# Kernel optimization log

Measured on AMD Instinct MI355X. Metric: run time of the kernel, lower is better.

The kernel has to match this reference:

```python
import jax, jax.numpy as jnp
import numpy as np
import math

D_MODEL = 1024
EXPAND = 2
D_INNER = EXPAND * D_MODEL        # 2048
HEADDIM = 64
NHEADS = D_INNER // HEADDIM       # 32
D_STATE = 128
D_CONV = 4
CHUNK = 128
SEQLEN = 4096
BATCH = 1                         # bidirectional merge in forward hard-codes batch=1
CONV_DIM = D_INNER + 2 * (2 * D_STATE)            # 2560
D_IN_PROJ = 2 * D_INNER + 2 * (2 * D_STATE) + 2 * NHEADS  # 4672
EPS = 1e-5


def silu(x):
    return x * jax.nn.sigmoid(x)


def segsum_exp(a):
    """exp(segsum(a)): out[..., i, j] = exp(sum_{k=j+1..i} a[..., k]) for i>=j else 0."""
    T = a.shape[-1]
    m1 = jnp.tril(jnp.ones((T, T), bool), -1)
    s = jnp.cumsum(jnp.where(m1, a[..., :, None], 0.0), axis=-2)
    m0 = jnp.tril(jnp.ones((T, T), bool))
    return jnp.where(m0, jnp.exp(jnp.where(m0, s, 0.0)), 0.0)


def ssd(x, A, B, C, chunk):
    """x:(b,L,h,p) A:(b,L,h) B,C:(b,L,n) (head dim of size 1 squeezed). L % chunk == 0."""
    b, L, h, p = x.shape
    c = L // chunk
    x = x.reshape(b, c, chunk, h, p)
    A = A.reshape(b, c, chunk, h).transpose(0, 3, 1, 2)   # (b,h,c,l)
    B = B.reshape(b, c, chunk, -1)
    C = C.reshape(b, c, chunk, -1)
    A_cs = jnp.cumsum(A, axis=-1)                          # (b,h,c,l)
    Lmat = segsum_exp(A)                                   # (b,h,c,l,l)
    # intra-chunk (diagonal block) outputs
    Y_diag = jnp.einsum('bcln,bcsn,bhcls,bcshp->bclhp', C, B, Lmat, x)
    # per-chunk states
    decay_states = jnp.exp(A_cs[..., -1:] - A_cs)          # (b,h,c,l)
    states = jnp.einsum('bcln,bhcl,bclhp->bchpn', B, decay_states, x)
    states = jnp.concatenate([jnp.zeros_like(states[:, :1]), states], axis=1)
    # inter-chunk recurrence via segsum over chunk boundaries
    decay_chunk = segsum_exp(jnp.pad(A_cs[..., -1], ((0, 0), (0, 0), (1, 0))))  # (b,h,c+1,c+1)
    new_states = jnp.einsum('bhzc,bchpn->bzhpn', decay_chunk, states)
    states, final_state = new_states[:, :-1], new_states[:, -1]
    Y_off = jnp.einsum('bcln,bchpn,bhcl->bclhp', C, states, jnp.exp(A_cs))
    Y = (Y_diag + Y_off).reshape(b, L, h, p)
    return Y, final_state


def setup_inputs() -> dict:
    key = jax.random.key(0)
    ks = jax.random.split(key, 8)
    s = 0.02
    u = jax.random.normal(ks[0], (BATCH, SEQLEN, D_MODEL), jnp.float32)
    in_proj_w = jax.random.normal(ks[1], (D_IN_PROJ, D_MODEL), jnp.float32) * s
    conv_w = jax.random.normal(ks[2], (CONV_DIM, 1, D_CONV), jnp.float32) * (1.0 / math.sqrt(D_CONV))
    conv_b = jnp.zeros((CONV_DIM,), jnp.float32)
    dt = jnp.exp(jax.random.uniform(ks[3], (NHEADS,)) * (math.log(0.1) - math.log(0.001)) + math.log(0.001))
    dt = jnp.clip(dt, 1e-4)
    dt_bias = dt + jnp.log(-jnp.expm1(-dt))
    A_log = jnp.log(jax.random.uniform(ks[4], (NHEADS,), minval=1.0, maxval=16.0))
    D = jnp.ones((NHEADS,), jnp.float32)
    fc_D_w = jax.random.normal(ks[5], (NHEADS, D_INNER), jnp.float32) * s
    norm_w = jnp.ones((D_INNER,), jnp.float32)
    out_proj_w = jax.random.normal(ks[6], (D_MODEL, D_INNER), jnp.float32) * s
    return dict(u=u, in_proj_w=in_proj_w, conv_w=conv_w, conv_b=conv_b, dt_bias=dt_bias,
                A_log=A_log, D=D, fc_D_w=fc_D_w, norm_w=norm_w, out_proj_w=out_proj_w)


def reference(u, in_proj_w, conv_w, conv_b, dt_bias, A_log, D, fc_D_w, norm_w, out_proj_w):
    b, l, _ = u.shape
    zxbcdt = u @ in_proj_w.T                               # (b,l,D_IN_PROJ)
    z = zxbcdt[..., :D_INNER]
    xBC = zxbcdt[..., D_INNER:D_INNER + CONV_DIM]
    dt = zxbcdt[..., D_INNER + CONV_DIM:]                  # (b,l,2*nheads)
    # fwd heads + time-reversed bwd heads stacked on batch dim
    dt = jnp.concatenate([dt[..., :NHEADS], jnp.flip(dt[..., NHEADS:], axis=1)], axis=0)
    dt = jax.nn.softplus(dt + dt_bias)                     # (2b,l,nheads)
    # depthwise causal conv1d + silu
    xc = jnp.transpose(xBC, (0, 2, 1))                     # (b,CONV_DIM,l)
    xc = jax.lax.conv_general_dilated(xc, conv_w, (1,), [(D_CONV - 1, 0)],
                                      feature_group_count=CONV_DIM,
                                      dimension_numbers=('NCH', 'OIH', 'NCH'))
    xc = xc + conv_b[None, :, None]
    xBC = silu(jnp.transpose(xc, (0, 2, 1)))               # (b,l,CONV_DIM)
    x = xBC[..., :D_INNER]
    BC = xBC[..., D_INNER:]
    x_og = x
    x2 = jnp.concatenate([x, jnp.flip(x, 1)], axis=0)      # (2b,l,d_inner)
    BC = jnp.concatenate([BC[..., :2 * D_STATE], jnp.flip(BC[..., 2 * D_STATE:], 1)], axis=0)
    B = BC[..., :D_STATE]
    C = BC[..., D_STATE:]
    xh = x2.reshape(2 * b, l, NHEADS, HEADDIM)
    A = -jnp.exp(A_log)
    Y, final_state = ssd(xh * dt[..., None], A * dt, B, C, CHUNK)
    y = Y + xh * D[:, None]
    y = y.reshape(2 * b, l, D_INNER)
    # torch.roll(shift=1, dim=1) then zero first step == shift right with zero pad
    y = jnp.concatenate([jnp.zeros_like(y[:, :1]), y[:, :-1]], axis=1)
    y_fw, y_bw = y[:b], jnp.flip(y[b:], 1)
    fd = x_og @ fc_D_w.T + D                               # F.linear(x_og, fc_D.weight, bias=D)
    y = y_fw + y_bw + x_og * jnp.repeat(fd, HEADDIM, axis=-1)
    # gated RMSNorm
    yg = y * silu(z)
    yn = yg * jax.lax.rsqrt(jnp.mean(yg * yg, axis=-1, keepdims=True) + EPS) * norm_w
    return yn @ out_proj_w.T
```

## Files before the change

kernel.cpp:

```cpp
#include <hip/hip_runtime.h>
#include <hip/hip_bf16.h>
#include <math.h>

#define L_SEQ   4096
#define DMODEL  1024
#define DINNER  2048
#define NHEADS  32
#define HEADDIM 64
#define DSTATE  128
#define NCHUNK  32
#define CHUNKL  128
#define CONVDIM 2560
#define DPROJ   4672
#define NPAD1   4736

typedef __hip_bfloat16 bf16;
__device__ __forceinline__ float b2f(bf16 x) { return __bfloat162float(x); }
__device__ __forceinline__ bf16 f2b(float x) { return __float2bfloat16(x); }
__device__ __forceinline__ float sh2f(short s) {
  return __uint_as_float(((unsigned int)(unsigned short)s) << 16);
}
__device__ __forceinline__ short f2bs(float x) {
  bf16 t = __float2bfloat16(x);
  return *reinterpret_cast<short*>(&t);
}

typedef __attribute__((ext_vector_type(8))) short bf16x8v;
typedef __attribute__((ext_vector_type(4))) float f32x4v;

__device__ __forceinline__ float dot8(bf16x8v x, float4 w0, float4 w1) {
  return sh2f(x[0]) * w0.x + sh2f(x[1]) * w0.y + sh2f(x[2]) * w0.z + sh2f(x[3]) * w0.w +
         sh2f(x[4]) * w1.x + sh2f(x[5]) * w1.y + sh2f(x[6]) * w1.z + sh2f(x[7]) * w1.w;
}


__global__ __launch_bounds__(256) void cast2_kernel(
    const float* __restrict__ u, const float* __restrict__ w1,
    bf16* __restrict__ u_bf, bf16* __restrict__ w1_bf) {
  const int NU = (L_SEQ * DMODEL) / 256;
  int bid = blockIdx.x;
  if (bid < NU) {
    int i = bid * 256 + threadIdx.x;
    u_bf[i] = f2b(u[i]);
  } else {
    int i = (bid - NU) * 256 + threadIdx.x;
    w1_bf[i] = (i < DPROJ * DMODEL) ? f2b(w1[i]) : f2b(0.f);
  }
}

__global__ __launch_bounds__(256) void cast_kernel(
    const float* __restrict__ src, bf16* __restrict__ dst, int n_src, int n_tot) {
  int i = blockIdx.x * 256 + threadIdx.x;
  if (i < n_tot) dst[i] = (i < n_src) ? f2b(src[i]) : f2b(0.f);
}

template <typename TC>
__global__ __launch_bounds__(256) void gemm_mfma(
    const bf16* __restrict__ A, int lda,
    const bf16* __restrict__ B, int ldb,
    TC* __restrict__ C, int ldc,
    int N, int K, int gridM, int gridN, int swz) {
  __shared__ short As[128][32];
  __shared__ short Bs[128][32];
  int tid = threadIdx.x;
  int lane = tid & 63;
  int w = tid >> 6;
  int wr = w >> 1, wc = w & 1;
  int bid = blockIdx.x;
  int bm, bn;
  if (swz) {
    int mst = gridM >> 3;
    int xk = bid & 7, q = bid >> 3;
    bm = (xk + 8 * (q % mst)) * 128;
    bn = (q / mst) * 128;
  } else {
    bm = (bid / gridN) * 128;
    bn = (bid % gridN) * 128;
  }
  f32x4v acc[4][4];
#pragma unroll
  for (int i = 0; i < 4; i++)
#pragma unroll
    for (int j = 0; j < 4; j++) acc[i][j] = (f32x4v){0.f, 0.f, 0.f, 0.f};

  const bf16* Ab = A + (size_t)(bm + w * 32 + (lane >> 2)) * lda + (lane & 3) * 8;
  const bf16* Bb = B + (size_t)(bn + w * 32 + (lane >> 2)) * ldb + (lane & 3) * 8;

  for (int k0 = 0; k0 < K; k0 += 32) {
    __builtin_amdgcn_global_load_lds(
        (const __attribute__((address_space(1))) void*)(Ab + k0),
        (__attribute__((address_space(3))) void*)&As[w * 32][0], 16, 0, 0);
    __builtin_amdgcn_global_load_lds(
        (const __attribute__((address_space(1))) void*)(Ab + (size_t)16 * lda + k0),
        (__attribute__((address_space(3))) void*)&As[w * 32 + 16][0], 16, 0, 0);
    __builtin_amdgcn_global_load_lds(
        (const __attribute__((address_space(1))) void*)(Bb + k0),
        (__attribute__((address_space(3))) void*)&Bs[w * 32][0], 16, 0, 0);
    __builtin_amdgcn_global_load_lds(
        (const __attribute__((address_space(1))) void*)(Bb + (size_t)16 * ldb + k0),
        (__attribute__((address_space(3))) void*)&Bs[w * 32 + 16][0], 16, 0, 0);
    __syncthreads();
    bf16x8v af[4], bv[4];
#pragma unroll
    for (int i = 0; i < 4; i++)
      af[i] = *(const bf16x8v*)&As[wr * 64 + i * 16 + (lane & 15)][(lane >> 4) * 8];
#pragma unroll
    for (int j = 0; j < 4; j++)
      bv[j] = *(const bf16x8v*)&Bs[wc * 64 + j * 16 + (lane & 15)][(lane >> 4) * 8];
#pragma unroll
    for (int i = 0; i < 4; i++)
#pragma unroll
      for (int j = 0; j < 4; j++)
        acc[i][j] = __builtin_amdgcn_mfma_f32_16x16x32_bf16(af[i], bv[j], acc[i][j], 0, 0, 0);
    __syncthreads();
  }
  int quad = lane >> 4;
  int cn = lane & 15;
#pragma unroll
  for (int i = 0; i < 4; i++) {
#pragma unroll
    for (int j = 0; j < 4; j++) {
      int col = bn + wc * 64 + j * 16 + cn;
      if (col < N) {
#pragma unroll
        for (int r = 0; r < 4; r++) {
          int row = bm + wr * 64 + i * 16 + quad * 4 + r;
          float v = acc[i][j][r];
          if constexpr (sizeof(TC) == 2) C[(size_t)row * ldc + col] = f2b(v);
          else                           C[(size_t)row * ldc + col] = v;
        }
      }
    }
  }
}

__global__ __launch_bounds__(256) void fc_kernel(
    const bf16* __restrict__ xbc, const float* __restrict__ Wf,
    const float* __restrict__ Dp, float* __restrict__ fd) {
  int lane = threadIdx.x & 63;
  int w = threadIdx.x >> 6;
  int t0 = (blockIdx.x * 4 + w) * 4;
  int h = lane & 31;
  int g = lane >> 5;
  const float* wr = Wf + (size_t)h * DINNER + g * 1024;
  const bf16* xr = xbc + (size_t)t0 * CONVDIM + g * 1024;
  float a0 = 0.f, a1 = 0.f, a2 = 0.f, a3 = 0.f;
  for (int k = 0; k < 1024; k += 8) {
    float4 w0 = *(const float4*)(wr + k);
    float4 w1 = *(const float4*)(wr + k + 4);
    bf16x8v x0 = *(const bf16x8v*)(xr + k);
    bf16x8v x1 = *(const bf16x8v*)(xr + CONVDIM + k);
    bf16x8v x2 = *(const bf16x8v*)(xr + 2 * CONVDIM + k);
    bf16x8v x3 = *(const bf16x8v*)(xr + 3 * CONVDIM + k);
    a0 += dot8(x0, w0, w1);
    a1 += dot8(x1, w0, w1);
    a2 += dot8(x2, w0, w1);
    a3 += dot8(x3, w0, w1);
  }
  a0 += __shfl_down(a0, 32);
  a1 += __shfl_down(a1, 32);
  a2 += __shfl_down(a2, 32);
  a3 += __shfl_down(a3, 32);
  if (lane < 32) {
    float d = Dp[h];
    fd[(t0 + 0) * NHEADS + h] = a0 + d;
    fd[(t0 + 1) * NHEADS + h] = a1 + d;
    fd[(t0 + 2) * NHEADS + h] = a2 + d;
    fd[(t0 + 3) * NHEADS + h] = a3 + d;
  }
}

#define CONV_BLOCKS ((L_SEQ / 4) * CONVDIM / 256)
__global__ __launch_bounds__(256) void conv_dt_kernel(
    const bf16* __restrict__ zx, const float* __restrict__ conv_w,
    const float* __restrict__ conv_b, bf16* __restrict__ xbc,
    const float* __restrict__ dt_bias, float* __restrict__ dt2) {
  int bid = blockIdx.x;
  if (bid < CONV_BLOCKS) {
    int idx = bid * 256 + threadIdx.x;
    int ch = idx % CONVDIM;
    int t0 = (idx / CONVDIM) * 4;
    const bf16* col = zx + DINNER + ch;
    float w0 = conv_w[ch * 4 + 0], w1 = conv_w[ch * 4 + 1];
    float w2 = conv_w[ch * 4 + 2], w3 = conv_w[ch * 4 + 3];
    float bsv = conv_b[ch];
    float x[7];
#pragma unroll
    for (int i = 0; i < 7; i++) {
      int t = t0 - 3 + i;
      x[i] = (t >= 0) ? b2f(col[(size_t)t * DPROJ]) : 0.f;
    }
#pragma unroll
    for (int j = 0; j < 4; j++) {
      float acc = bsv + w0 * x[j] + w1 * x[j + 1] + w2 * x[j + 2] + w3 * x[j + 3];
      xbc[(size_t)(t0 + j) * CONVDIM + ch] = f2b(acc / (1.f + __expf(-acc)));
    }
  } else {
    int idx = (bid - CONV_BLOCKS) * 256 + threadIdx.x;
    int h = idx % NHEADS;
    int t = (idx / NHEADS) % L_SEQ;
    int b = idx / (NHEADS * L_SEQ);
    float v;
    if (b == 0) v = b2f(zx[(size_t)t * DPROJ + 4608 + h]);
    else        v = b2f(zx[(size_t)(L_SEQ - 1 - t) * DPROJ + 4608 + NHEADS + h]);
    v += dt_bias[h];
    dt2[idx] = (v > 20.f) ? v : log1pf(expf(v));
  }
}

__global__ __launch_bounds__(256) void gmat_kernel(
    const bf16* __restrict__ xbc, bf16* __restrict__ G) {
  __shared__ bf16 Cs[32][136];
  __shared__ bf16 Bs[128][136];
  int blk = blockIdx.x;
  int quarter = blk & 3;
  int bc = blk >> 2;
  int b = bc / NCHUNK, c = bc % NCHUNK;
  int l0 = quarter * 32;
  int tid = threadIdx.x;
  int lane = tid & 63;
  int w = tid >> 6;
  int bofs = b ? 2304 : 2048;
  int cofs = b ? 2432 : 2176;
  for (int o = tid; o < CHUNKL * DSTATE / 8; o += 256) {
    int s = o >> 4;
    int n8 = (o & 15) * 8;
    int t = b ? (L_SEQ - 1 - (c * CHUNKL + s)) : (c * CHUNKL + s);
    *(bf16x8v*)&Bs[s][n8] = *(const bf16x8v*)&xbc[(size_t)t * CONVDIM + bofs + n8];
  }
  for (int o = tid; o < 32 * DSTATE / 8; o += 256) {
    int l = o >> 4;
    int n8 = (o & 15) * 8;
    int t = b ? (L_SEQ - 1 - (c * CHUNKL + l0 + l)) : (c * CHUNKL + l0 + l);
    *(bf16x8v*)&Cs[l][n8] = *(const bf16x8v*)&xbc[(size_t)t * CONVDIM + cofs + n8];
  }
  __syncthreads();
  if (w > quarter) return;
  f32x4v acc[2][2];
#pragma unroll
  for (int i = 0; i < 2; i++)
#pragma unroll
    for (int j = 0; j < 2; j++) acc[i][j] = (f32x4v){0.f, 0.f, 0.f, 0.f};
#pragma unroll
  for (int k0 = 0; k0 < 128; k0 += 32) {
    bf16x8v a0 = *(const bf16x8v*)&Cs[(lane & 15)][(lane >> 4) * 8 + k0];
    bf16x8v a1 = *(const bf16x8v*)&Cs[16 + (lane & 15)][(lane >> 4) * 8 + k0];
#pragma unroll
    for (int j = 0; j < 2; j++) {
      bf16x8v bv = *(const bf16x8v*)&Bs[(2 * w + j) * 16 + (lane & 15)][(lane >> 4) * 8 + k0];
      acc[0][j] = __builtin_amdgcn_mfma_f32_16x16x32_bf16(a0, bv, acc[0][j], 0, 0, 0);
      acc[1][j] = __builtin_amdgcn_mfma_f32_16x16x32_bf16(a1, bv, acc[1][j], 0, 0, 0);
    }
  }
  int quad = lane >> 4, cn = lane & 15;
  bf16* Gb = G + (size_t)bc * CHUNKL * CHUNKL;
#pragma unroll
  for (int i = 0; i < 2; i++)
#pragma unroll
    for (int j = 0; j < 2; j++)
#pragma unroll
      for (int r = 0; r < 4; r++) {
        int l = l0 + i * 16 + quad * 4 + r;
        int s = (2 * w + j) * 16 + cn;
        Gb[l * CHUNKL + s] = f2b(acc[i][j][r]);
      }
}

__global__ __launch_bounds__(256) void chunk_kernel(
    const bf16* __restrict__ xbc, const float* __restrict__ dt2,
    const float* __restrict__ A_log,
    bf16* __restrict__ states, float* __restrict__ csum) {
  int gid = blockIdx.x;
  int h = gid % NHEADS;
  int bc = gid / NHEADS;
  int c = bc % NCHUNK, b = bc / NCHUNK;
  int tid = threadIdx.x;
  int lane = tid & 63;
  int w = tid >> 6;
  __shared__ bf16 BdT[128][136];
  __shared__ bf16 xdtT[64][136];
  __shared__ float acs[CHUNKL];
  __shared__ float dtl[CHUNKL];
  __shared__ float decays[CHUNKL];
  if (tid < CHUNKL)
    dtl[tid] = dt2[((size_t)b * L_SEQ + c * CHUNKL + tid) * NHEADS + h];
  __syncthreads();
  if (tid == 0) {
    float Ah = -__expf(A_log[h]);
    float s = 0.f;
    for (int l = 0; l < CHUNKL; l++) { s += Ah * dtl[l]; acs[l] = s; }
    csum[gid] = __expf(s);
  }
  __syncthreads();
  if (tid < CHUNKL) decays[tid] = __expf(acs[CHUNKL - 1] - acs[tid]);
  for (int o = tid; o < CHUNKL * HEADDIM / 8; o += 256) {
    int s = o & 127;
    int p8 = (o >> 7) * 8;
    int t = b ? (L_SEQ - 1 - (c * CHUNKL + s)) : (c * CHUNKL + s);
    bf16x8v xv = *(const bf16x8v*)&xbc[(size_t)t * CONVDIM + h * HEADDIM + p8];
    float d = dtl[s];
#pragma unroll
    for (int j = 0; j < 8; j++) xdtT[p8 + j][s] = f2b(sh2f(xv[j]) * d);
  }
  __syncthreads();
  for (int o = tid; o < CHUNKL * CHUNKL / 8; o += 256) {
    int l = o & 127;
    int n8 = (o >> 7) * 8;
    int t = b ? (L_SEQ - 1 - (c * CHUNKL + l)) : (c * CHUNKL + l);
    bf16x8v bv = *(const bf16x8v*)&xbc[(size_t)t * CONVDIM + (b ? 2304 : 2048) + n8];
    float d = decays[l];
#pragma unroll
    for (int j = 0; j < 8; j++) BdT[n8 + j][l] = f2b(sh2f(bv[j]) * d);
  }
  __syncthreads();
  f32x4v accS[8];
#pragma unroll
  for (int j = 0; j < 8; j++) accS[j] = (f32x4v){0.f, 0.f, 0.f, 0.f};
#pragma unroll
  for (int k0 = 0; k0 < 128; k0 += 32) {
    bf16x8v av = *(const bf16x8v*)&xdtT[w * 16 + (lane & 15)][(lane >> 4) * 8 + k0];
#pragma unroll
    for (int j = 0; j < 8; j++) {
      bf16x8v bv = *(const bf16x8v*)&BdT[j * 16 + (lane & 15)][(lane >> 4) * 8 + k0];
      accS[j] = __builtin_amdgcn_mfma_f32_16x16x32_bf16(av, bv, accS[j], 0, 0, 0);
    }
  }
  int quad = lane >> 4, cn = lane & 15;
  bf16* st = states + (size_t)gid * (HEADDIM * DSTATE);
#pragma unroll
  for (int j = 0; j < 8; j++)
#pragma unroll
    for (int r = 0; r < 4; r++) {
      int p = w * 16 + quad * 4 + r;
      int n = j * 16 + cn;
      st[p * DSTATE + n] = f2b(accS[j][r]);
    }
}

__global__ __launch_bounds__(256) void scan_kernel(
    bf16* __restrict__ states, const float* __restrict__ csum) {
  int idx = blockIdx.x * 256 + threadIdx.x;
  int n = idx % DSTATE;
  int p = (idx / DSTATE) % HEADDIM;
  int h = (idx / (DSTATE * HEADDIM)) % NHEADS;
  int b = idx / (DSTATE * HEADDIM * NHEADS);
  size_t base = ((size_t)(b * NCHUNK) * NHEADS + h) * (HEADDIM * DSTATE) + p * DSTATE + n;
  const size_t cstride = (size_t)NHEADS * HEADDIM * DSTATE;
  float tmp[NCHUNK], cv[NCHUNK];
#pragma unroll
  for (int c = 0; c < NCHUNK; c++) tmp[c] = b2f(states[base + c * cstride]);
#pragma unroll
  for (int c = 0; c < NCHUNK; c++) cv[c] = csum[(b * NCHUNK + c) * NHEADS + h];
  float S = 0.f;
#pragma unroll
  for (int c = 0; c < NCHUNK; c++) {
    states[base + c * cstride] = f2b(S);
    S = cv[c] * S + tmp[c];
  }
}

__global__ __launch_bounds__(256) void yoff_kernel(
    const bf16* __restrict__ xbc, const float* __restrict__ dt2,
    const float* __restrict__ A_log, const bf16* __restrict__ G,
    const bf16* __restrict__ states, const float* __restrict__ Dp,
    bf16* __restrict__ Y) {
  int gid = blockIdx.x;
  int h = gid % NHEADS;
  int bc = gid / NHEADS;
  int c = bc % NCHUNK, b = bc / NCHUNK;
  int tid = threadIdx.x;
  int lane = tid & 63;
  int w = tid >> 6;
  __shared__ bf16 WB[128][136];
  __shared__ bf16 SX[64][136];
  __shared__ float acs[CHUNKL];
  __shared__ float dtl[CHUNKL];
  __shared__ float eAl[CHUNKL];
  if (tid < CHUNKL)
    dtl[tid] = dt2[((size_t)b * L_SEQ + c * CHUNKL + tid) * NHEADS + h];
  __syncthreads();
  if (tid == 0) {
    float Ah = -__expf(A_log[h]);
    float s = 0.f;
    for (int l = 0; l < CHUNKL; l++) { s += Ah * dtl[l]; acs[l] = s; }
  }
  __syncthreads();
  if (tid < CHUNKL) eAl[tid] = __expf(acs[tid]);
  for (int o = tid; o < CHUNKL * HEADDIM / 8; o += 256) {
    int s = o & 127;
    int p8 = (o >> 7) * 8;
    int t = b ? (L_SEQ - 1 - (c * CHUNKL + s)) : (c * CHUNKL + s);
    bf16x8v xv = *(const bf16x8v*)&xbc[(size_t)t * CONVDIM + h * HEADDIM + p8];
    float d = dtl[s];
#pragma unroll
    for (int j = 0; j < 8; j++) SX[p8 + j][s] = f2b(sh2f(xv[j]) * d);
  }
  {
    const bf16* Gb = G + (size_t)bc * CHUNKL * CHUNKL;
    for (int o = tid; o < CHUNKL * CHUNKL / 8; o += 256) {
      int l = o >> 4;
      int s8 = (o & 15) * 8;
      bf16x8v g = *(const bf16x8v*)&Gb[l * CHUNKL + s8];
      float al = acs[l];
      bf16x8v wv;
#pragma unroll
      for (int j = 0; j < 8; j++) {
        int s = s8 + j;
        float e = (s <= l) ? sh2f(g[j]) * __expf(al - acs[s]) : 0.f;
        wv[j] = f2bs(e);
      }
      *(bf16x8v*)&WB[l][s8] = wv;
    }
  }
  __syncthreads();
  f32x4v accY[2][4];
#pragma unroll
  for (int i = 0; i < 2; i++)
#pragma unroll
    for (int j = 0; j < 4; j++) accY[i][j] = (f32x4v){0.f, 0.f, 0.f, 0.f};
#pragma unroll
  for (int k0 = 0; k0 < 128; k0 += 32) {
    bf16x8v a0 = *(const bf16x8v*)&WB[w * 32 + (lane & 15)][(lane >> 4) * 8 + k0];
    bf16x8v a1 = *(const bf16x8v*)&WB[w * 32 + 16 + (lane & 15)][(lane >> 4) * 8 + k0];
#pragma unroll
    for (int j = 0; j < 4; j++) {
      bf16x8v bv = *(const bf16x8v*)&SX[j * 16 + (lane & 15)][(lane >> 4) * 8 + k0];
      accY[0][j] = __builtin_amdgcn_mfma_f32_16x16x32_bf16(a0, bv, accY[0][j], 0, 0, 0);
      accY[1][j] = __builtin_amdgcn_mfma_f32_16x16x32_bf16(a1, bv, accY[1][j], 0, 0, 0);
    }
  }
  __syncthreads();
  {
    int cofs = b ? 2432 : 2176;
    for (int o = tid; o < CHUNKL * DSTATE / 8; o += 256) {
      int l = o >> 4;
      int n8 = (o & 15) * 8;
      int t = b ? (L_SEQ - 1 - (c * CHUNKL + l)) : (c * CHUNKL + l);
      bf16x8v cv = *(const bf16x8v*)&xbc[(size_t)t * CONVDIM + cofs + n8];
      float e = eAl[l];
      bf16x8v ov;
#pragma unroll
      for (int j = 0; j < 8; j++) ov[j] = f2bs(sh2f(cv[j]) * e);
      *(bf16x8v*)&WB[l][n8] = ov;
    }
    const bf16* stp = states + (size_t)gid * (HEADDIM * DSTATE);
    for (int o = tid; o < HEADDIM * DSTATE / 8; o += 256) {
      int p = o >> 4;
      int n8 = (o & 15) * 8;
      *(bf16x8v*)&SX[p][n8] = *(const bf16x8v*)&stp[o * 8];
    }
  }
  __syncthreads();
#pragma unroll
  for (int k0 = 0; k0 < 128; k0 += 32) {
    bf16x8v a0 = *(const bf16x8v*)&WB[w * 32 + (lane & 15)][(lane >> 4) * 8 + k0];
    bf16x8v a1 = *(const bf16x8v*)&WB[w * 32 + 16 + (lane & 15)][(lane >> 4) * 8 + k0];
#pragma unroll
    for (int j = 0; j < 4; j++) {
      bf16x8v bv = *(const bf16x8v*)&SX[j * 16 + (lane & 15)][(lane >> 4) * 8 + k0];
      accY[0][j] = __builtin_amdgcn_mfma_f32_16x16x32_bf16(a0, bv, accY[0][j], 0, 0, 0);
      accY[1][j] = __builtin_amdgcn_mfma_f32_16x16x32_bf16(a1, bv, accY[1][j], 0, 0, 0);
    }
  }
  int quad = lane >> 4, cn = lane & 15;
  float Dh = Dp[h];
#pragma unroll
  for (int i = 0; i < 2; i++)
#pragma unroll
    for (int j = 0; j < 4; j++)
#pragma unroll
      for (int r = 0; r < 4; r++) {
        int l = w * 32 + i * 16 + quad * 4 + r;
        int p = j * 16 + cn;
        int t = b ? (L_SEQ - 1 - (c * CHUNKL + l)) : (c * CHUNKL + l);
        float xv = b2f(xbc[(size_t)t * CONVDIM + h * HEADDIM + p]);
        size_t yi = ((size_t)b * L_SEQ + c * CHUNKL + l) * DINNER + h * HEADDIM + p;
        Y[yi] = f2b(accY[i][j][r] + xv * Dh);
      }
}

__global__ __launch_bounds__(256) void combine_kernel(
    const bf16* __restrict__ Y, const bf16* __restrict__ xbc,
    const bf16* __restrict__ zx, const float* __restrict__ fd,
    const float* __restrict__ norm_w, bf16* __restrict__ yn) {
  int t = blockIdx.x;
  int tid = threadIdx.x;
  int j8 = tid * 8;
  float yf[8], yb[8];
#pragma unroll
  for (int j = 0; j < 8; j++) { yf[j] = 0.f; yb[j] = 0.f; }
  if (t >= 1) {
    bf16x8v v = *(const bf16x8v*)&Y[(size_t)(t - 1) * DINNER + j8];
#pragma unroll
    for (int j = 0; j < 8; j++) yf[j] = sh2f(v[j]);
  }
  if (t <= L_SEQ - 2) {
    bf16x8v v = *(const bf16x8v*)&Y[((size_t)L_SEQ + (L_SEQ - 2 - t)) * DINNER + j8];
#pragma unroll
    for (int j = 0; j < 8; j++) yb[j] = sh2f(v[j]);
  }
  bf16x8v xogv = *(const bf16x8v*)&xbc[(size_t)t * CONVDIM + j8];
  bf16x8v zv = *(const bf16x8v*)&zx[(size_t)t * DPROJ + j8];
  float fdv = fd[t * NHEADS + (j8 >> 6)];
  float yg[8];
  float ss = 0.f;
#pragma unroll
  for (int j = 0; j < 8; j++) {
    float y = yf[j] + yb[j] + sh2f(xogv[j]) * fdv;
    float z = sh2f(zv[j]);
    float g = y * (z / (1.f + __expf(-z)));
    yg[j] = g;
    ss += g * g;
  }
#pragma unroll
  for (int off = 32; off > 0; off >>= 1) ss += __shfl_down(ss, off);
  __shared__ float red[4];
  if ((tid & 63) == 0) red[tid >> 6] = ss;
  __syncthreads();
  float tot = red[0] + red[1] + red[2] + red[3];
  float scale = rsqrtf(tot / (float)DINNER + 1e-5f);
  float4 nw0 = *(const float4*)&norm_w[j8];
  float4 nw1 = *(const float4*)&norm_w[j8 + 4];
  bf16x8v ov;
  ov[0] = f2bs(yg[0] * scale * nw0.x);
  ov[1] = f2bs(yg[1] * scale * nw0.y);
  ov[2] = f2bs(yg[2] * scale * nw0.z);
  ov[3] = f2bs(yg[3] * scale * nw0.w);
  ov[4] = f2bs(yg[4] * scale * nw1.x);
  ov[5] = f2bs(yg[5] * scale * nw1.y);
  ov[6] = f2bs(yg[6] * scale * nw1.z);
  ov[7] = f2bs(yg[7] * scale * nw1.w);
  *(bf16x8v*)&yn[(size_t)t * DINNER + j8] = ov;
}

extern "C" void kernel_launch(void* const* d_in, const int* in_sizes, int n_in,
                              void* d_out, int out_size, void* d_ws, size_t ws_size,
                              hipStream_t stream) {
  const float* u         = (const float*)d_in[0];
  const float* in_proj_w = (const float*)d_in[1];
  const float* conv_w    = (const float*)d_in[2];
  const float* conv_b    = (const float*)d_in[3];
  const float* dt_bias   = (const float*)d_in[4];
  const float* A_log     = (const float*)d_in[5];
  const float* Dp        = (const float*)d_in[6];
  const float* fc_D_w    = (const float*)d_in[7];
  const float* norm_w    = (const float*)d_in[8];
  const float* out_proj_w= (const float*)d_in[9];
  float* out = (float*)d_out;

  char* base = (char*)d_ws;
  bf16*  zx  = (bf16*)base;  base += (size_t)L_SEQ * DPROJ * 2;
  bf16*  xbc = (bf16*)base;  base += (size_t)L_SEQ * CONVDIM * 2;
  float* dt2 = (float*)base; base += (size_t)2 * L_SEQ * NHEADS * 4;
  bf16*  G   = (bf16*)base;  base += (size_t)2 * NCHUNK * CHUNKL * CHUNKL * 4;
  bf16*  Yb  = (bf16*)base;  base += (size_t)2 * L_SEQ * DINNER * 4;
  bf16*  stb = (bf16*)base;  base += (size_t)2 * NCHUNK * NHEADS * HEADDIM * DSTATE * 4;
  float* cs  = (float*)base; base += (size_t)2 * NCHUNK * NHEADS * 4;
  bf16*  u_bf   = (bf16*)Yb;
  bf16*  w1p_bf = (bf16*)((char*)Yb + 9437184);
  bf16*  w2_bf  = (bf16*)G;
  bf16*  yn     = (bf16*)stb;
  float* fd     = (float*)((char*)stb + 33554432);

  cast2_kernel<<<(L_SEQ * DMODEL + NPAD1 * DMODEL) / 256, 256, 0, stream>>>(
      u, in_proj_w, u_bf, w1p_bf);
  gemm_mfma<bf16><<<(L_SEQ / 128) * (NPAD1 / 128), 256, 0, stream>>>(
      u_bf, DMODEL, w1p_bf, DMODEL, zx, DPROJ, DPROJ, DMODEL,
      L_SEQ / 128, NPAD1 / 128, 0);
  conv_dt_kernel<<<CONV_BLOCKS + (2 * L_SEQ * NHEADS) / 256, 256, 0, stream>>>(
      zx, conv_w, conv_b, xbc, dt_bias, dt2);
  gmat_kernel<<<2 * NCHUNK * 4, 256, 0, stream>>>(xbc, G);
  chunk_kernel<<<2 * NCHUNK * NHEADS, 256, 0, stream>>>(
      xbc, dt2, A_log, stb, cs);
  scan_kernel<<<(2 * NHEADS * HEADDIM * DSTATE) / 256, 256, 0, stream>>>(stb, cs);
  yoff_kernel<<<2 * NCHUNK * NHEADS, 256, 0, stream>>>(
      xbc, dt2, A_log, G, stb, Dp, Yb);
  cast_kernel<<<(DMODEL * DINNER + 255) / 256, 256, 0, stream>>>(
      out_proj_w, w2_bf, DMODEL * DINNER, DMODEL * DINNER);
  fc_kernel<<<L_SEQ / 16, 256, 0, stream>>>(xbc, fc_D_w, Dp, fd);
  combine_kernel<<<L_SEQ, 256, 0, stream>>>(Yb, xbc, zx, fd, norm_w, yn);
  gemm_mfma<float><<<(L_SEQ / 128) * (DMODEL / 128), 256, 0, stream>>>(
      yn, DINNER, w2_bf, DINNER, out, DMODEL, DMODEL, DINNER,
      L_SEQ / 128, DMODEL / 128, 1);
}
```

Measured before the change: 407.5 us.

## Replace in-projection GEMM with 256x256 tiled, 8-phase pipelined MFMA kernel

Replaces the generic 128x128 MFMA GEMM for the input projection with a dedicated 512-thread kernel using 256x256 output tiles. It uses direct global-to-LDS loads, double-buffered swizzled shared memory and an interleaved schedule of LDS reads, async stages and MFMA bursts with priority hints. The aim is more data reuse per tile and better overlap of memory traffic with matrix math. The weight padding grows to 4864 columns, so the last column tile wastes work, and the large LDS footprint limits occupancy.

```diff
diff --git a/kernel.cpp b/kernel.cpp
--- a/kernel.cpp
+++ b/kernel.cpp
@@ -12,7 +12,7 @@
 #define CHUNKL  128
 #define CONVDIM 2560
 #define DPROJ   4672
-#define NPAD1   4736
+#define NPAD2   4864
 
 typedef __hip_bfloat16 bf16;
 __device__ __forceinline__ float b2f(bf16 x) { return __bfloat162float(x); }
@@ -52,6 +52,151 @@
     const float* __restrict__ src, bf16* __restrict__ dst, int n_src, int n_tot) {
   int i = blockIdx.x * 256 + threadIdx.x;
   if (i < n_tot) dst[i] = (i < n_src) ? f2b(src[i]) : f2b(0.f);
+}
+
+#define G1_K  1024
+#define G1_GN 19
+#define G1_NT (G1_K / 64)
+
+__global__ __launch_bounds__(512, 2) void gemm1_8ph(
+    const bf16* __restrict__ A, const bf16* __restrict__ B, bf16* __restrict__ C) {
+  __shared__ bf16 Al[2][2][8192];
+  __shared__ bf16 Bl[2][2][8192];
+  const int tid = threadIdx.x;
+  const int lane = tid & 63;
+  const int w = tid >> 6;
+  const int wm = w >> 2;
+  const int wn = w & 3;
+  const int bm = (blockIdx.x / G1_GN) * 256;
+  const int bn = (blockIdx.x % G1_GN) * 256;
+  const int scol = ((lane & 3) ^ (((lane >> 5) & 1) << 1)) * 8;
+  const int cin = ((lane >> 4) * 8) ^ (((lane >> 3) & 1) << 4);
+  const int r16 = lane & 15;
+  const bf16* Ag = A + (size_t)bm * G1_K;
+  const bf16* Bg = B + (size_t)bn * G1_K;
+
+  auto stage = [&](int mat, int tt, int hf) {
+    const bf16* g = (mat ? Bg : Ag)
+        + (size_t)(hf * 128 + (w >> 1) * 16 + (lane >> 2)) * G1_K
+        + tt * 64 + (w & 1) * 32 + scol;
+    bf16* d0 = mat ? &Bl[tt & 1][hf][0] : &Al[tt & 1][hf][0];
+    __builtin_amdgcn_global_load_lds(
+        (const __attribute__((address_space(1))) void*)g,
+        (__attribute__((address_space(3))) void*)(d0 + w * 512), 16, 0, 0);
+    __builtin_amdgcn_global_load_lds(
+        (const __attribute__((address_space(1))) void*)(g + (size_t)64 * G1_K),
+        (__attribute__((address_space(3))) void*)(d0 + (8 + w) * 512), 16, 0, 0);
+  };
+
+  f32x4v acc[8][4];
+#pragma unroll
+  for (int i = 0; i < 8; i++)
+#pragma unroll
+    for (int j = 0; j < 4; j++) acc[i][j] = (f32x4v){0.f, 0.f, 0.f, 0.f};
+
+  stage(0, 0, 0); stage(0, 0, 1); stage(1, 0, 0); stage(1, 0, 1);
+  stage(0, 1, 0); stage(0, 1, 1); stage(1, 1, 0);
+  asm volatile("s_waitcnt vmcnt(6)" ::: "memory");
+  __builtin_amdgcn_s_barrier();
+  __builtin_amdgcn_sched_barrier(0);
+
+#pragma unroll 2
+  for (int t = 0; t < G1_NT; ++t) {
+    const int slot = t & 1;
+    const bf16* Ah = &Al[slot][wm][0];
+    const bf16* Bh = &Bl[slot][wn >> 1][0];
+    const int brb = (wn & 1) * 4;
+    bf16x8v a[4][2], b[4][2];
+#pragma unroll
+    for (int i = 0; i < 4; i++) {
+      a[i][0] = *(const bf16x8v*)&Ah[(i * 2 + 0) * 512 + r16 * 32 + cin];
+      a[i][1] = *(const bf16x8v*)&Ah[(i * 2 + 1) * 512 + r16 * 32 + cin];
+    }
+#pragma unroll
+    for (int j = 0; j < 2; j++) {
+      b[j][0] = *(const bf16x8v*)&Bh[((brb + j) * 2 + 0) * 512 + r16 * 32 + cin];
+      b[j][1] = *(const bf16x8v*)&Bh[((brb + j) * 2 + 1) * 512 + r16 * 32 + cin];
+    }
+    if (t + 1 < G1_NT) stage(1, t + 1, 1);
+    __builtin_amdgcn_s_barrier();
+    asm volatile("s_waitcnt lgkmcnt(0)" ::: "memory");
+    __builtin_amdgcn_s_setprio(1);
+#pragma unroll
+    for (int i = 0; i < 4; i++)
+#pragma unroll
+      for (int j = 0; j < 2; j++) {
+        acc[i][j] = __builtin_amdgcn_mfma_f32_16x16x32_bf16(a[i][0], b[j][0], acc[i][j], 0, 0, 0);
+        acc[i][j] = __builtin_amdgcn_mfma_f32_16x16x32_bf16(a[i][1], b[j][1], acc[i][j], 0, 0, 0);
+      }
+    __builtin_amdgcn_s_setprio(0);
+    __builtin_amdgcn_s_barrier();
+#pragma unroll
+    for (int j = 2; j < 4; j++) {
+      b[j][0] = *(const bf16x8v*)&Bh[((brb + j) * 2 + 0) * 512 + r16 * 32 + cin];
+      b[j][1] = *(const bf16x8v*)&Bh[((brb + j) * 2 + 1) * 512 + r16 * 32 + cin];
+    }
+    __builtin_amdgcn_s_barrier();
+    asm volatile("s_waitcnt lgkmcnt(0)" ::: "memory");
+    __builtin_amdgcn_s_setprio(1);
+#pragma unroll
+    for (int i = 0; i < 4; i++)
+#pragma unroll
+      for (int j = 2; j < 4; j++) {
+        acc[i][j] = __builtin_amdgcn_mfma_f32_16x16x32_bf16(a[i][0], b[j][0], acc[i][j], 0, 0, 0);
+        acc[i][j] = __builtin_amdgcn_mfma_f32_16x16x32_bf16(a[i][1], b[j][1], acc[i][j], 0, 0, 0);
+      }
+    __builtin_amdgcn_s_setprio(0);
+    __builtin_amdgcn_s_barrier();
+#pragma unroll
+    for (int i = 0; i < 4; i++) {
+      a[i][0] = *(const bf16x8v*)&Ah[((4 + i) * 2 + 0) * 512 + r16 * 32 + cin];
+      a[i][1] = *(const bf16x8v*)&Ah[((4 + i) * 2 + 1) * 512 + r16 * 32 + cin];
+    }
+    if (t + 2 < G1_NT) stage(1, t + 2, 0);
+    __builtin_amdgcn_s_barrier();
+    asm volatile("s_waitcnt lgkmcnt(0)" ::: "memory");
+    __builtin_amdgcn_s_setprio(1);
+#pragma unroll
+    for (int i = 0; i < 4; i++)
+#pragma unroll
+      for (int j = 2; j < 4; j++) {
+        acc[4 + i][j] = __builtin_amdgcn_mfma_f32_16x16x32_bf16(a[i][0], b[j][0], acc[4 + i][j], 0, 0, 0);
+        acc[4 + i][j] = __builtin_amdgcn_mfma_f32_16x16x32_bf16(a[i][1], b[j][1], acc[4 + i][j], 0, 0, 0);
+      }
+    __builtin_amdgcn_s_setprio(0);
+    __builtin_amdgcn_s_barrier();
+    if (t + 2 < G1_NT) { stage(0, t + 2, 0); stage(0, t + 2, 1); }
+    __builtin_amdgcn_s_barrier();
+    __builtin_amdgcn_s_setprio(1);
+#pragma unroll
+    for (int i = 0; i < 4; i++)
+#pragma unroll
+      for (int j = 0; j < 2; j++) {
+        acc[4 + i][j] = __builtin_amdgcn_mfma_f32_16x16x32_bf16(a[i][0], b[j][0], acc[4 + i][j], 0, 0, 0);
+        acc[4 + i][j] = __builtin_amdgcn_mfma_f32_16x16x32_bf16(a[i][1], b[j][1], acc[4 + i][j], 0, 0, 0);
+      }
+    __builtin_amdgcn_s_setprio(0);
+    if (t < G1_NT - 2)       asm volatile("s_waitcnt vmcnt(6)" ::: "memory");
+    else if (t == G1_NT - 2) asm volatile("s_waitcnt vmcnt(0)" ::: "memory");
+    __builtin_amdgcn_s_barrier();
+    __builtin_amdgcn_sched_barrier(0);
+  }
+
+  const int quad = lane >> 4;
+  const int cn = lane & 15;
+#pragma unroll
+  for (int i = 0; i < 8; i++)
+#pragma unroll
+    for (int j = 0; j < 4; j++) {
+      int col = bn + wn * 64 + j * 16 + cn;
+      if (col < DPROJ) {
+#pragma unroll
+        for (int r = 0; r < 4; r++) {
+          int row = bm + wm * 128 + i * 16 + quad * 4 + r;
+          C[(size_t)row * DPROJ + col] = f2b(acc[i][j][r]);
+        }
+      }
+    }
 }
 
 template <typename TC>
@@ -562,11 +707,9 @@
   bf16*  yn     = (bf16*)stb;
   float* fd     = (float*)((char*)stb + 33554432);
 
-  cast2_kernel<<<(L_SEQ * DMODEL + NPAD1 * DMODEL) / 256, 256, 0, stream>>>(
+  cast2_kernel<<<(L_SEQ * DMODEL + NPAD2 * DMODEL) / 256, 256, 0, stream>>>(
       u, in_proj_w, u_bf, w1p_bf);
-  gemm_mfma<bf16><<<(L_SEQ / 128) * (NPAD1 / 128), 256, 0, stream>>>(
-      u_bf, DMODEL, w1p_bf, DMODEL, zx, DPROJ, DPROJ, DMODEL,
-      L_SEQ / 128, NPAD1 / 128, 0);
+  gemm1_8ph<<<(L_SEQ / 256) * G1_GN, 512, 0, stream>>>(u_bf, w1p_bf, zx);
   conv_dt_kernel<<<CONV_BLOCKS + (2 * L_SEQ * NHEADS) / 256, 256, 0, stream>>>(
       zx, conv_w, conv_b, xbc, dt_bias, dt2);
   gmat_kernel<<<2 * NCHUNK * 4, 256, 0, stream>>>(xbc, G);
```

Result: no change. 415.0 us (+1.8%).
